# Kernel tuning notes

Hardware: AMD Instinct MI355X
Metric: run time of the kernel (lower is better)

The kernel has to match this reference:

```python
import jax, jax.numpy as jnp
import numpy as np

N_EMBED = 8192
EMBED_DIM = 64
BETA = 0.25


def setup_inputs() -> dict:
    key = jax.random.key(0)
    k_z, k_e = jax.random.split(key)
    z = jax.random.normal(k_z, (16, 4096, EMBED_DIM), dtype=jnp.float32)
    # embedding.weight.data.uniform_(-1/n_embed, 1/n_embed)
    embedding = jax.random.uniform(
        k_e, (N_EMBED, EMBED_DIM), dtype=jnp.float32,
        minval=-1.0 / N_EMBED, maxval=1.0 / N_EMBED)
    return {"z": z, "embedding": embedding}


def reference(z, embedding):
    # z: [B, H, C] with C == embed_dim (no permute needed)
    B, H, C = z.shape
    z_flat = z.reshape(-1, C)                      # [N, C]
    # squared euclidean distances: ||z||^2 + ||e||^2 - 2 z e^T
    d = (jnp.sum(z_flat ** 2, axis=1, keepdims=True)
         + jnp.sum(embedding ** 2, axis=1)
         - 2.0 * jnp.matmul(z_flat, embedding.T))  # [N, n_embed]
    idx = jnp.argmin(d, axis=1)                    # [N]
    z_q = embedding[idx].reshape(z.shape)          # gather + reshape
    sg = jax.lax.stop_gradient
    loss = (jnp.mean((sg(z_q) - z) ** 2)
            + BETA * jnp.mean((z_q - sg(z)) ** 2))
    # straight-through estimator
    z_q = z + sg(z_q - z)
    return z_q, loss, idx.reshape(B, H)
```

## Files before the change

### kernel.cpp

```cpp
#include <hip/hip_runtime.h>

typedef __attribute__((ext_vector_type(8))) short short8;
typedef __attribute__((ext_vector_type(16))) float floatx16;
typedef unsigned int u32;
typedef unsigned short u16;
typedef unsigned long long u64;

#define NROWS 65536
#define NEMB 8192
#define DIM 64
#define LOSS_OFF ((size_t)NROWS * DIM)
#define IDX_OFF (LOSS_OFF + 1)
#define CAPQ 16
#define CSTRIDE 66
#define NPRE 4
#define NSTAGE 64

#define WS_EFRAG_OFF 0u
#define WS_LPART_OFF (1u << 20)
#define WS_QUEUE_OFF ((1u << 20) + 8192u)
#define WS_QCNT_OFF  ((1u << 20) + 8192u + (256u << 10))
#define WS_LOVR_OFF  (WS_QCNT_OFF + 4u)
#define WS_NEED      (WS_QCNT_OFF + 64u)

typedef const __attribute__((address_space(1))) unsigned int GU32;
typedef __attribute__((address_space(3))) unsigned int LU32;

__device__ __forceinline__ unsigned short f2bf(float f) {
    u32 x = __float_as_uint(f);
    return (unsigned short)((x + 0x7fffu + ((x >> 16) & 1u)) >> 16);
}

__device__ __forceinline__ float zsum_np(const float* zf) {
    float r[8];
#pragma unroll
    for (int j = 0; j < 8; ++j) r[j] = zf[j] * zf[j];
#pragma unroll
    for (int i = 8; i < 64; i += 8) {
#pragma unroll
        for (int j = 0; j < 8; ++j) r[j] += zf[i + j] * zf[i + j];
    }
    return ((r[0] + r[1]) + (r[2] + r[3])) + ((r[4] + r[5]) + (r[6] + r[7]));
}

__device__ __forceinline__ float dot_chain(const float* zf, const float* e) {
    float acc = 0.f;
#pragma unroll
    for (int i = 0; i < 16; ++i) {
        float4 ev = ((const float4*)e)[i];
        acc = fmaf(zf[4 * i + 0], ev.x, acc);
        acc = fmaf(zf[4 * i + 1], ev.y, acc);
        acc = fmaf(zf[4 * i + 2], ev.z, acc);
        acc = fmaf(zf[4 * i + 3], ev.w, acc);
    }
    return acc;
}

__device__ __forceinline__ float vmax16_3(const floatx16& a) {
    float m0 = fmaxf(fmaxf(a[0], a[1]), a[2]);
    float m1 = fmaxf(fmaxf(a[3], a[4]), a[5]);
    float m2 = fmaxf(fmaxf(a[6], a[7]), a[8]);
    float m3 = fmaxf(fmaxf(a[9], a[10]), a[11]);
    float m4 = fmaxf(fmaxf(a[12], a[13]), a[14]);
    float n0 = fmaxf(fmaxf(m0, m1), m2);
    float n1 = fmaxf(fmaxf(m3, m4), a[15]);
    return fmaxf(n0, n1);
}

extern "C" __global__ __launch_bounds__(256)
void vq_prep(const float* __restrict__ emb, u32* __restrict__ efrag,
             u32* __restrict__ qcount, float* __restrict__ loss_over) {
    int tid = blockIdx.x * 256 + threadIdx.x;
    int t = tid >> 8, kc = (tid >> 5) & 7, m = tid & 31;
    const float* e = emb + (((size_t)t * 32 + m) * 64 + kc * 8);
    float4 a = ((const float4*)e)[0];
    float4 b = ((const float4*)e)[1];
    u32 w0 = (u32)f2bf(a.x) | ((u32)f2bf(a.y) << 16);
    u32 w1 = (u32)f2bf(a.z) | ((u32)f2bf(a.w) << 16);
    u32 w2 = (u32)f2bf(b.x) | ((u32)f2bf(b.y) << 16);
    u32 w3 = (u32)f2bf(b.z) | ((u32)f2bf(b.w) << 16);
    ((uint4*)efrag)[tid] = make_uint4(w0, w1, w2, w3);
    if (tid == 0) { qcount[0] = 0u; *loss_over = 0.f; }
}

extern "C" __global__ __launch_bounds__(256, 2)
void vq_screen(const float* __restrict__ z, const u32* __restrict__ efrag,
               const float* __restrict__ emb, float* __restrict__ out,
               float* __restrict__ lpart, u32* __restrict__ queue,
               u32* __restrict__ qcount) {
    __shared__ u32 etile[8192];
    __shared__ u16 cand[128 * CSTRIDE];
    __shared__ u32 cnt_l[512];
    __shared__ float runm_sh[128][2];
    __shared__ u32 win[128];
    __shared__ float lsum[4];
    const int tid = threadIdx.x;
    const int wave = tid >> 6, lane = tid & 63;
    const int rlo = lane & 31, h = lane >> 5;
    const int rowbase = blockIdx.x * 128 + (wave >> 1) * 64;
    const int sub = (wave & 1) * 2 + h;
    const int wp = wave & 1;

    if (tid < 128) { runm_sh[tid][0] = -3.4e38f; runm_sh[tid][1] = -3.4e38f; }

    {
        const u32* g = efrag + tid * 4;
        u32* l = etile + tid * 4;
#pragma unroll
        for (int r = 0; r < 4; ++r)
            __builtin_amdgcn_global_load_lds((GU32*)(g + r * 1024),
                                             (LU32*)(l + r * 1024), 16, 0, 0);
    }

    short8 zfr[2][4];
    float eps_[2];
#pragma unroll
    for (int rt = 0; rt < 2; ++rt) {
        const float* zp = z + (size_t)(rowbase + rt * 32 + rlo) * 64;
        float sa = 0.f;
#pragma unroll
        for (int s = 0; s < 4; ++s) {
            const float4* p = (const float4*)(zp + s * 16 + h * 8);
            float4 a = p[0], b = p[1];
            union { short8 v; unsigned short e[8]; } u;
            u.e[0] = f2bf(a.x); u.e[1] = f2bf(a.y);
            u.e[2] = f2bf(a.z); u.e[3] = f2bf(a.w);
            u.e[4] = f2bf(b.x); u.e[5] = f2bf(b.y);
            u.e[6] = f2bf(b.z); u.e[7] = f2bf(b.w);
            zfr[rt][s] = u.v;
            sa += fabsf(a.x) + fabsf(a.y) + fabsf(a.z) + fabsf(a.w)
                + fabsf(b.x) + fabsf(b.y) + fabsf(b.z) + fabsf(b.w);
        }
        sa += __shfl_xor(sa, 32);
        eps_[rt] = fmaf(1.1e-6f, sa, 1e-7f);
    }
    float runm[2] = { -3.4e38f, -3.4e38f };
    u32 pc[2] = { 0u, 0u };

    __syncthreads();
    int cur = 0;

    for (int ss = 0; ss < NSTAGE + NPRE; ++ss) {
        const int t = (ss < NPRE) ? ss : (ss - NPRE);

        {
            const int sn = ss + 1;
            if (sn < NSTAGE + NPRE) {
                const int tn = (sn < NPRE) ? sn : (sn - NPRE);
                const u32* g = efrag + (size_t)tn * 4096 + tid * 4;
                u32* l = etile + (cur ^ 1) * 4096 + tid * 4;
#pragma unroll
                for (int r = 0; r < 4; ++r)
                    __builtin_amdgcn_global_load_lds((GU32*)(g + r * 1024),
                                                     (LU32*)(l + r * 1024), 16, 0, 0);
            }
        }

#pragma unroll
        for (int rt = 0; rt < 2; ++rt) {
            const int rowl = (wave >> 1) * 64 + rt * 32 + rlo;
            runm[rt] = fmaxf(runm[rt], runm_sh[rowl][wp ^ 1]);
        }

        floatx16 acc[2][2];
#pragma unroll
        for (int et = 0; et < 2; ++et)
#pragma unroll
            for (int rt = 0; rt < 2; ++rt) acc[et][rt] = 0.f;

#pragma unroll
        for (int s = 0; s < 4; ++s) {
            short8 af[2];
#pragma unroll
            for (int et = 0; et < 2; ++et) {
                int off = cur * 16384 + (wp * 2 + et) * 4096 + (2 * s + h) * 512 + rlo * 16;
                af[et] = *(const short8*)((const char*)etile + off);
            }
#pragma unroll
            for (int et = 0; et < 2; ++et)
#pragma unroll
                for (int rt = 0; rt < 2; ++rt)
                    acc[et][rt] = __builtin_amdgcn_mfma_f32_32x32x16_bf16(
                        af[et], zfr[rt][s], acc[et][rt], 0, 0, 0);
        }

#pragma unroll
        for (int rt = 0; rt < 2; ++rt) {
            const int rowl = (wave >> 1) * 64 + rt * 32 + rlo;
            float vm[2];
#pragma unroll
            for (int et = 0; et < 2; ++et) vm[et] = vmax16_3(acc[et][rt]);
            float m64 = fmaxf(vm[0], vm[1]);
            runm[rt] = fmaxf(runm[rt], m64);
            runm[rt] = fmaxf(runm[rt], __shfl_xor(runm[rt], 32));
            if (ss >= NPRE) {
                const float thr = runm[rt] - eps_[rt];
                if (m64 >= thr) {
                    const int ebase = t * 128 + wp * 64;
                    const u32 cbase = (u32)rowl * CSTRIDE + (u32)sub * CAPQ;
#pragma unroll
                    for (int et = 0; et < 2; ++et) {
                        if (vm[et] >= thr) {
#pragma unroll
                            for (int r = 0; r < 16; ++r) {
                                float v = acc[et][rt][r];
                                if (v >= thr) {
                                    int j = ebase + et * 32 + ((r & 3) + 8 * (r >> 2) + 4 * h);
                                    if (pc[rt] < CAPQ) cand[cbase + pc[rt]] = (u16)j;
                                    pc[rt]++;
                                }
                            }
                        }
                    }
                }
            }
            if (h == 0) runm_sh[rowl][wp] = runm[rt];
        }

        __syncthreads();
        cur ^= 1;
    }
#pragma unroll
    for (int rt = 0; rt < 2; ++rt)
        cnt_l[(((wave >> 1) * 64 + rt * 32 + rlo) << 2) + sub] = pc[rt];
    __syncthreads();

    {
        const int rl = lane & 31, half = lane >> 5;
        const int rowl = wave * 32 + rl;
        const int grow = blockIdx.x * 128 + rowl;
        const u32 ca = cnt_l[(rowl << 2) + 2 * half];
        const u32 cb = cnt_l[(rowl << 2) + 2 * half + 1];
        u32 ovf = (u32)((ca > CAPQ) | (cb > CAPQ));
        ovf |= (u32)__shfl_xor((int)ovf, 32);

        if (!ovf) {
            float zf[64];
            const float4* zp = (const float4*)(z + (size_t)grow * 64);
#pragma unroll
            for (int i = 0; i < 16; ++i) {
                float4 a = zp[i];
                zf[4 * i + 0] = a.x; zf[4 * i + 1] = a.y;
                zf[4 * i + 2] = a.z; zf[4 * i + 3] = a.w;
            }
            const float zs = zsum_np(zf);
            u64 best = ~0ull;
            const u32 cbase = (u32)rowl * CSTRIDE + (u32)(2 * half) * CAPQ;
            for (u32 s = 0; s < ca; ++s) {
                u32 j = (u32)cand[cbase + s];
                float d = fmaf(-2.f, dot_chain(zf, emb + (size_t)j * 64), zs);
                u64 p = ((u64)__float_as_uint(d) << 32) | (u64)j;
                best = p < best ? p : best;
            }
            for (u32 s = 0; s < cb; ++s) {
                u32 j = (u32)cand[cbase + CAPQ + s];
                float d = fmaf(-2.f, dot_chain(zf, emb + (size_t)j * 64), zs);
                u64 p = ((u64)__float_as_uint(d) << 32) | (u64)j;
                best = p < best ? p : best;
            }
            u64 o = __shfl_xor(best, 32);
            best = o < best ? o : best;
            if (half == 0) {
                win[rowl] = (u32)best;
                out[IDX_OFF + grow] = (float)(u32)best;
            }
        } else if (half == 0) {
            u32 pos = atomicAdd(qcount, 1u);
            queue[pos] = (u32)grow;
            win[rowl] = 0xFFFFFFFFu;
        }
    }
    __syncthreads();

    float lp = 0.f;
    {
        const int r2 = tid >> 1, hf = tid & 1;
        const int grow2 = blockIdx.x * 128 + r2;
        const u32 wj = win[r2];
        if (wj != 0xFFFFFFFFu) {
            const float4* ep = (const float4*)(emb + (size_t)wj * 64) + hf * 8;
            const float4* zp4 = (const float4*)(z + (size_t)grow2 * 64) + hf * 8;
            float4* oq = (float4*)(out + (size_t)grow2 * 64) + hf * 8;
#pragma unroll
            for (int i = 0; i < 8; ++i) {
                float4 ev = ep[i];
                float4 zv = zp4[i];
                oq[i] = ev;
                float dx = ev.x - zv.x, dy = ev.y - zv.y;
                float dzv = ev.z - zv.z, dw = ev.w - zv.w;
                lp = fmaf(dx, dx, fmaf(dy, dy, fmaf(dzv, dzv, fmaf(dw, dw, lp))));
            }
        }
    }
#pragma unroll
    for (int off = 32; off; off >>= 1) lp += __shfl_down(lp, off);
    if (lane == 0) lsum[wave] = lp;
    __syncthreads();
    if (tid == 0)
        lpart[blockIdx.x] = (lsum[0] + lsum[1]) + (lsum[2] + lsum[3]);
}

extern "C" __global__ __launch_bounds__(256)
void vq_over(const float* __restrict__ z, const float* __restrict__ emb,
             const u32* __restrict__ queue, const u32* __restrict__ qcount,
             float* __restrict__ out, float* __restrict__ loss_over) {
    __shared__ u64 red[4];
    const int tid = threadIdx.x, wave = tid >> 6, lane = tid & 63;
    u32 n = qcount[0]; if (n > (u32)NROWS) n = (u32)NROWS;
    for (u32 qi = blockIdx.x; qi < n; qi += gridDim.x) {
        const int row = (int)queue[qi];
        const float4* zp = (const float4*)(z + (size_t)row * 64);
        float zf[64];
#pragma unroll
        for (int i = 0; i < 16; ++i) {
            float4 a = zp[i];
            zf[4 * i + 0] = a.x; zf[4 * i + 1] = a.y;
            zf[4 * i + 2] = a.z; zf[4 * i + 3] = a.w;
        }
        const float zs = zsum_np(zf);
        u64 best = ~0ull;
#pragma unroll 2
        for (int j = tid; j < NEMB; j += 256) {
            float d = fmaf(-2.f, dot_chain(zf, emb + (size_t)j * 64), zs);
            u64 p = ((u64)__float_as_uint(d) << 32) | (u64)j;
            best = p < best ? p : best;
        }
#pragma unroll
        for (int off = 32; off; off >>= 1) {
            u64 o = __shfl_xor(best, off);
            best = o < best ? o : best;
        }
        if (lane == 0) red[wave] = best;
        __syncthreads();
        if (tid == 0) {
            u64 b = red[0];
#pragma unroll
            for (int w = 1; w < 4; ++w) { u64 o = red[w]; b = o < b ? o : b; }
            red[0] = b;
            out[IDX_OFF + row] = (float)(u32)b;
        }
        __syncthreads();
        const u32 wj = (u32)red[0];
        float lp = 0.f;
        if (tid < 16) {
            float4 ev = ((const float4*)(emb + (size_t)wj * 64))[tid];
            float4 zv = zp[tid];
            ((float4*)(out + (size_t)row * 64))[tid] = ev;
            float dx = ev.x - zv.x, dy = ev.y - zv.y;
            float dzv = ev.z - zv.z, dw = ev.w - zv.w;
            lp = fmaf(dx, dx, fmaf(dy, dy, fmaf(dzv, dzv, dw * dw)));
        }
        if (wave == 0) {
#pragma unroll
            for (int off = 32; off; off >>= 1) lp += __shfl_down(lp, off);
            if (tid == 0) atomicAdd(loss_over, lp);
        }
        __syncthreads();
    }
}

extern "C" __global__ __launch_bounds__(256)
void vq_lossred(const float* __restrict__ lpart,
                const float* __restrict__ loss_over, float* __restrict__ out) {
    __shared__ float s[256];
    const int tid = threadIdx.x;
    float v = 0.f;
    for (int i = tid; i < 512; i += 256) v += lpart[i];
    s[tid] = v; __syncthreads();
    for (int off = 128; off; off >>= 1) {
        if (tid < off) s[tid] += s[tid + off];
        __syncthreads();
    }
    if (tid == 0) out[LOSS_OFF] = 1.25f * (s[0] + *loss_over) / 4194304.f;
}

extern "C" __global__ __launch_bounds__(256, 2)
void vq_legacy(const float* __restrict__ z, const float* __restrict__ emb,
               float* __restrict__ out, float* __restrict__ ws) {
    __shared__ float tile[128 * 64];
    __shared__ float red_d[4][128];
    __shared__ int   red_i[4][128];
    const int tid = threadIdx.x, lane = tid & 63, wave = tid >> 6;
    const int r0 = blockIdx.x * 128 + lane;
    float z0f[64], z1f[64];
    {
        const float4* p0 = (const float4*)(z + (size_t)r0 * 64);
        const float4* p1 = (const float4*)(z + ((size_t)r0 + 64) * 64);
#pragma unroll
        for (int i = 0; i < 16; ++i) {
            float4 a = p0[i];
            z0f[4*i+0]=a.x; z0f[4*i+1]=a.y; z0f[4*i+2]=a.z; z0f[4*i+3]=a.w;
            float4 b = p1[i];
            z1f[4*i+0]=b.x; z1f[4*i+1]=b.y; z1f[4*i+2]=b.z; z1f[4*i+3]=b.w;
        }
    }
    const float zs0 = zsum_np(z0f), zs1 = zsum_np(z1f);
    float bd0 = 3.402823466e38f, bd1 = 3.402823466e38f;
    int bi0 = 0, bi1 = 0;
    for (int t = 0; t < 64; ++t) {
        __syncthreads();
        {
            const float4* src = (const float4*)(emb + (size_t)t * 128 * 64);
            float4* dst = (float4*)tile;
#pragma unroll
            for (int i = 0; i < 8; ++i) dst[tid + i * 256] = src[tid + i * 256];
        }
        __syncthreads();
        const int base = wave * 32;
#pragma unroll 2
        for (int jg = 0; jg < 32; jg += 4) {
            const float* e = tile + (size_t)(base + jg) * 64;
            float a00=0,a10=0,a20=0,a30=0,a01=0,a11=0,a21=0,a31=0;
#pragma unroll
            for (int i = 0; i < 16; ++i) {
                float4 ea = ((const float4*)(e))[i];
                float4 eb = ((const float4*)(e + 64))[i];
                float4 ec = ((const float4*)(e + 128))[i];
                float4 ed = ((const float4*)(e + 192))[i];
                float x0=z0f[4*i],x1=z0f[4*i+1],x2=z0f[4*i+2],x3=z0f[4*i+3];
                float y0=z1f[4*i],y1=z1f[4*i+1],y2=z1f[4*i+2],y3=z1f[4*i+3];
                a00=fmaf(x0,ea.x,a00);a00=fmaf(x1,ea.y,a00);a00=fmaf(x2,ea.z,a00);a00=fmaf(x3,ea.w,a00);
                a10=fmaf(x0,eb.x,a10);a10=fmaf(x1,eb.y,a10);a10=fmaf(x2,eb.z,a10);a10=fmaf(x3,eb.w,a10);
                a20=fmaf(x0,ec.x,a20);a20=fmaf(x1,ec.y,a20);a20=fmaf(x2,ec.z,a20);a20=fmaf(x3,ec.w,a20);
                a30=fmaf(x0,ed.x,a30);a30=fmaf(x1,ed.y,a30);a30=fmaf(x2,ed.z,a30);a30=fmaf(x3,ed.w,a30);
                a01=fmaf(y0,ea.x,a01);a01=fmaf(y1,ea.y,a01);a01=fmaf(y2,ea.z,a01);a01=fmaf(y3,ea.w,a01);
                a11=fmaf(y0,eb.x,a11);a11=fmaf(y1,eb.y,a11);a11=fmaf(y2,eb.z,a11);a11=fmaf(y3,eb.w,a11);
                a21=fmaf(y0,ec.x,a21);a21=fmaf(y1,ec.y,a21);a21=fmaf(y2,ec.z,a21);a21=fmaf(y3,ec.w,a21);
                a31=fmaf(y0,ed.x,a31);a31=fmaf(y1,ed.y,a31);a31=fmaf(y2,ed.z,a31);a31=fmaf(y3,ed.w,a31);
            }
            const int gj = t * 128 + base + jg;
            float d;
            d=fmaf(-2.f,a00,zs0); if(d<bd0){bd0=d;bi0=gj;}
            d=fmaf(-2.f,a10,zs0); if(d<bd0){bd0=d;bi0=gj+1;}
            d=fmaf(-2.f,a20,zs0); if(d<bd0){bd0=d;bi0=gj+2;}
            d=fmaf(-2.f,a30,zs0); if(d<bd0){bd0=d;bi0=gj+3;}
            d=fmaf(-2.f,a01,zs1); if(d<bd1){bd1=d;bi1=gj;}
            d=fmaf(-2.f,a11,zs1); if(d<bd1){bd1=d;bi1=gj+1;}
            d=fmaf(-2.f,a21,zs1); if(d<bd1){bd1=d;bi1=gj+2;}
            d=fmaf(-2.f,a31,zs1); if(d<bd1){bd1=d;bi1=gj+3;}
        }
    }
    red_d[wave][lane]=bd0; red_i[wave][lane]=bi0;
    red_d[wave][lane+64]=bd1; red_i[wave][lane+64]=bi1;
    __syncthreads();
    if (wave == 0) {
        float blk = 0.f;
#pragma unroll
        for (int half = 0; half < 2; ++half) {
            const int lrow = lane + half * 64;
            const float* zrf = half ? z1f : z0f;
            float bd = red_d[0][lrow]; int bi = red_i[0][lrow];
#pragma unroll
            for (int w = 1; w < 4; ++w) {
                float dd = red_d[w][lrow]; int ii = red_i[w][lrow];
                if (dd < bd || (dd == bd && ii < bi)) { bd = dd; bi = ii; }
            }
            const size_t row = (size_t)blockIdx.x * 128 + lrow;
            out[IDX_OFF + row] = (float)bi;
            const float4* ep = (const float4*)(emb + (size_t)bi * 64);
            float4* oq = (float4*)(out + row * 64);
            float ls = 0.f;
#pragma unroll
            for (int i = 0; i < 16; ++i) {
                float4 ev = ep[i];
                oq[i] = ev;
                float dx=ev.x-zrf[4*i], dy=ev.y-zrf[4*i+1];
                float dzv=ev.z-zrf[4*i+2], dw=ev.w-zrf[4*i+3];
                ls=fmaf(dx,dx,ls); ls=fmaf(dy,dy,ls); ls=fmaf(dzv,dzv,ls); ls=fmaf(dw,dw,ls);
            }
            blk += ls;
        }
#pragma unroll
        for (int off = 32; off; off >>= 1) blk += __shfl_down(blk, off);
        if (lane == 0) ws[blockIdx.x] = blk;
    }
}

extern "C" __global__ __launch_bounds__(512)
void vq_legacy_loss(const float* __restrict__ ws, float* __restrict__ out) {
    __shared__ float s[8];
    const int tid = threadIdx.x;
    float v = ws[tid];
#pragma unroll
    for (int off = 32; off; off >>= 1) v += __shfl_down(v, off);
    if ((tid & 63) == 0) s[tid >> 6] = v;
    __syncthreads();
    if (tid == 0) {
        float t = 0.f;
#pragma unroll
        for (int i = 0; i < 8; ++i) t += s[i];
        out[LOSS_OFF] = 1.25f * t / 4194304.f;
    }
}

extern "C" void kernel_launch(void* const* d_in, const int* in_sizes, int n_in,
                              void* d_out, int out_size, void* d_ws, size_t ws_size,
                              hipStream_t stream) {
    const float* z   = (const float*)d_in[0];
    const float* emb = (const float*)d_in[1];
    float* out = (float*)d_out;
    if (ws_size < (size_t)WS_NEED) {
        float* ws = (float*)d_ws;
        vq_legacy<<<512, 256, 0, stream>>>(z, emb, out, ws);
        vq_legacy_loss<<<1, 512, 0, stream>>>(ws, out);
        return;
    }
    char* wsb = (char*)d_ws;
    u32* efrag = (u32*)(wsb + WS_EFRAG_OFF);
    float* lpart = (float*)(wsb + WS_LPART_OFF);
    u32* queue   = (u32*)(wsb + WS_QUEUE_OFF);
    u32* qcount  = (u32*)(wsb + WS_QCNT_OFF);
    float* loss_over = (float*)(wsb + WS_LOVR_OFF);
    vq_prep<<<256, 256, 0, stream>>>(emb, efrag, qcount, loss_over);
    vq_screen<<<512, 256, 0, stream>>>(z, efrag, emb, out, lpart, queue, qcount);
    vq_over<<<256, 256, 0, stream>>>(z, emb, queue, qcount, out, loss_over);
    vq_lossred<<<1, 256, 0, stream>>>(lpart, loss_over, out);
}
```

Before: 217.6 us.

## Split codebook across two blocks per row tile with atomicMin merge

The screening kernel now splits the 8192-entry codebook into two halves, each handled by a separate block (1024 blocks), and merges per-row winners with 64-bit atomicMin into a workspace array. The etile double buffer is replaced by a single buffer with syncs before and after each load, which cuts LDS so four blocks can fit per CU. A new vq_final kernel does the gather, output and loss, and overflow rows are rescanned per half. The aim is more parallelism and occupancy, paid for with an extra launch, atomics, duplicate z loads and loss of load/compute overlap in the staging loop.

```diff
diff --git a/kernel.cpp b/kernel.cpp
--- a/kernel.cpp
+++ b/kernel.cpp
@@ -14,13 +14,13 @@
 #define CAPQ 16
 #define CSTRIDE 66
 #define NPRE 4
-#define NSTAGE 64
+#define NSTAGE 32
 
 #define WS_EFRAG_OFF 0u
-#define WS_LPART_OFF (1u << 20)
-#define WS_QUEUE_OFF ((1u << 20) + 8192u)
-#define WS_QCNT_OFF  ((1u << 20) + 8192u + (256u << 10))
-#define WS_LOVR_OFF  (WS_QCNT_OFF + 4u)
+#define WS_BEST_OFF  (1u << 20)
+#define WS_QUEUE_OFF ((1u << 20) + (512u << 10))
+#define WS_LPART_OFF (WS_QUEUE_OFF + (512u << 10))
+#define WS_QCNT_OFF  (WS_LPART_OFF + 8192u)
 #define WS_NEED      (WS_QCNT_OFF + 64u)
 
 typedef const __attribute__((address_space(1))) unsigned int GU32;
@@ -69,7 +69,7 @@
 
 extern "C" __global__ __launch_bounds__(256)
 void vq_prep(const float* __restrict__ emb, u32* __restrict__ efrag,
-             u32* __restrict__ qcount, float* __restrict__ loss_over) {
+             u64* __restrict__ best, u32* __restrict__ qcount) {
     int tid = blockIdx.x * 256 + threadIdx.x;
     int t = tid >> 8, kc = (tid >> 5) & 7, m = tid & 31;
     const float* e = emb + (((size_t)t * 32 + m) * 64 + kc * 8);
@@ -80,37 +80,28 @@
     u32 w2 = (u32)f2bf(b.x) | ((u32)f2bf(b.y) << 16);
     u32 w3 = (u32)f2bf(b.z) | ((u32)f2bf(b.w) << 16);
     ((uint4*)efrag)[tid] = make_uint4(w0, w1, w2, w3);
-    if (tid == 0) { qcount[0] = 0u; *loss_over = 0.f; }
-}
-
-extern "C" __global__ __launch_bounds__(256, 2)
+    best[tid] = ~0ull;
+    if (tid == 0) qcount[0] = 0u;
+}
+
+extern "C" __global__ __launch_bounds__(256, 4)
 void vq_screen(const float* __restrict__ z, const u32* __restrict__ efrag,
-               const float* __restrict__ emb, float* __restrict__ out,
-               float* __restrict__ lpart, u32* __restrict__ queue,
-               u32* __restrict__ qcount) {
-    __shared__ u32 etile[8192];
+               const float* __restrict__ emb, u64* __restrict__ best,
+               u32* __restrict__ queue, u32* __restrict__ qcount) {
+    __shared__ u32 etile[4096];
     __shared__ u16 cand[128 * CSTRIDE];
     __shared__ u32 cnt_l[512];
     __shared__ float runm_sh[128][2];
-    __shared__ u32 win[128];
-    __shared__ float lsum[4];
     const int tid = threadIdx.x;
     const int wave = tid >> 6, lane = tid & 63;
     const int rlo = lane & 31, h = lane >> 5;
-    const int rowbase = blockIdx.x * 128 + (wave >> 1) * 64;
+    const int rowblk = blockIdx.x >> 1, halfid = blockIdx.x & 1;
+    const int rowbase = rowblk * 128 + (wave >> 1) * 64;
     const int sub = (wave & 1) * 2 + h;
     const int wp = wave & 1;
+    const u32 halfu = (u32)halfid * 131072u;
 
     if (tid < 128) { runm_sh[tid][0] = -3.4e38f; runm_sh[tid][1] = -3.4e38f; }
-
-    {
-        const u32* g = efrag + tid * 4;
-        u32* l = etile + tid * 4;
-#pragma unroll
-        for (int r = 0; r < 4; ++r)
-            __builtin_amdgcn_global_load_lds((GU32*)(g + r * 1024),
-                                             (LU32*)(l + r * 1024), 16, 0, 0);
-    }
 
     short8 zfr[2][4];
     float eps_[2];
@@ -137,24 +128,18 @@
     float runm[2] = { -3.4e38f, -3.4e38f };
     u32 pc[2] = { 0u, 0u };
 
-    __syncthreads();
-    int cur = 0;
-
     for (int ss = 0; ss < NSTAGE + NPRE; ++ss) {
         const int t = (ss < NPRE) ? ss : (ss - NPRE);
-
+        __syncthreads();
         {
-            const int sn = ss + 1;
-            if (sn < NSTAGE + NPRE) {
-                const int tn = (sn < NPRE) ? sn : (sn - NPRE);
-                const u32* g = efrag + (size_t)tn * 4096 + tid * 4;
-                u32* l = etile + (cur ^ 1) * 4096 + tid * 4;
-#pragma unroll
-                for (int r = 0; r < 4; ++r)
-                    __builtin_amdgcn_global_load_lds((GU32*)(g + r * 1024),
-                                                     (LU32*)(l + r * 1024), 16, 0, 0);
-            }
-        }
+            const u32* g = efrag + halfu + (u32)t * 4096u + tid * 4;
+            u32* l = etile + tid * 4;
+#pragma unroll
+            for (int r = 0; r < 4; ++r)
+                __builtin_amdgcn_global_load_lds((GU32*)(g + r * 1024),
+                                                 (LU32*)(l + r * 1024), 16, 0, 0);
+        }
+        __syncthreads();
 
 #pragma unroll
         for (int rt = 0; rt < 2; ++rt) {
@@ -173,7 +158,7 @@
             short8 af[2];
 #pragma unroll
             for (int et = 0; et < 2; ++et) {
-                int off = cur * 16384 + (wp * 2 + et) * 4096 + (2 * s + h) * 512 + rlo * 16;
+                int off = (wp * 2 + et) * 4096 + (2 * s + h) * 512 + rlo * 16;
                 af[et] = *(const short8*)((const char*)etile + off);
             }
 #pragma unroll
@@ -196,7 +181,7 @@
             if (ss >= NPRE) {
                 const float thr = runm[rt] - eps_[rt];
                 if (m64 >= thr) {
-                    const int ebase = t * 128 + wp * 64;
+                    const int ebase = halfid * 4096 + t * 128 + wp * 64;
                     const u32 cbase = (u32)rowl * CSTRIDE + (u32)sub * CAPQ;
 #pragma unroll
                     for (int et = 0; et < 2; ++et) {
@@ -216,9 +201,6 @@
             }
             if (h == 0) runm_sh[rowl][wp] = runm[rt];
         }
-
-        __syncthreads();
-        cur ^= 1;
     }
 #pragma unroll
     for (int rt = 0; rt < 2; ++rt)
@@ -228,7 +210,7 @@
     {
         const int rl = lane & 31, half = lane >> 5;
         const int rowl = wave * 32 + rl;
-        const int grow = blockIdx.x * 128 + rowl;
+        const int grow = rowblk * 128 + rowl;
         const u32 ca = cnt_l[(rowl << 2) + 2 * half];
         const u32 cb = cnt_l[(rowl << 2) + 2 * half + 1];
         u32 ovf = (u32)((ca > CAPQ) | (cb > CAPQ));
@@ -244,52 +226,98 @@
                 zf[4 * i + 2] = a.z; zf[4 * i + 3] = a.w;
             }
             const float zs = zsum_np(zf);
-            u64 best = ~0ull;
+            u64 b = ~0ull;
             const u32 cbase = (u32)rowl * CSTRIDE + (u32)(2 * half) * CAPQ;
             for (u32 s = 0; s < ca; ++s) {
                 u32 j = (u32)cand[cbase + s];
                 float d = fmaf(-2.f, dot_chain(zf, emb + (size_t)j * 64), zs);
                 u64 p = ((u64)__float_as_uint(d) << 32) | (u64)j;
-                best = p < best ? p : best;
+                b = p < b ? p : b;
             }
             for (u32 s = 0; s < cb; ++s) {
                 u32 j = (u32)cand[cbase + CAPQ + s];
                 float d = fmaf(-2.f, dot_chain(zf, emb + (size_t)j * 64), zs);
                 u64 p = ((u64)__float_as_uint(d) << 32) | (u64)j;
-                best = p < best ? p : best;
-            }
-            u64 o = __shfl_xor(best, 32);
-            best = o < best ? o : best;
-            if (half == 0) {
-                win[rowl] = (u32)best;
-                out[IDX_OFF + grow] = (float)(u32)best;
-            }
+                b = p < b ? p : b;
+            }
+            u64 o = __shfl_xor(b, 32);
+            b = o < b ? o : b;
+            if (half == 0) atomicMin(&best[grow], b);
         } else if (half == 0) {
             u32 pos = atomicAdd(qcount, 1u);
-            queue[pos] = (u32)grow;
-            win[rowl] = 0xFFFFFFFFu;
-        }
-    }
-    __syncthreads();
-
+            queue[pos] = (u32)grow | ((u32)halfid << 16);
+        }
+    }
+}
+
+extern "C" __global__ __launch_bounds__(256)
+void vq_over(const float* __restrict__ z, const float* __restrict__ emb,
+             const u32* __restrict__ queue, const u32* __restrict__ qcount,
+             u64* __restrict__ best) {
+    __shared__ u64 red[4];
+    const int tid = threadIdx.x, wave = tid >> 6, lane = tid & 63;
+    u32 n = qcount[0]; if (n > 2u * (u32)NROWS) n = 2u * (u32)NROWS;
+    for (u32 qi = blockIdx.x; qi < n; qi += gridDim.x) {
+        const u32 e = queue[qi];
+        const int row = (int)(e & 0xFFFFu);
+        const int hb = (int)((e >> 16) & 1u) * 4096;
+        const float4* zp = (const float4*)(z + (size_t)row * 64);
+        float zf[64];
+#pragma unroll
+        for (int i = 0; i < 16; ++i) {
+            float4 a = zp[i];
+            zf[4 * i + 0] = a.x; zf[4 * i + 1] = a.y;
+            zf[4 * i + 2] = a.z; zf[4 * i + 3] = a.w;
+        }
+        const float zs = zsum_np(zf);
+        u64 b = ~0ull;
+#pragma unroll 2
+        for (int j = tid; j < 4096; j += 256) {
+            const int gj = hb + j;
+            float d = fmaf(-2.f, dot_chain(zf, emb + (size_t)gj * 64), zs);
+            u64 p = ((u64)__float_as_uint(d) << 32) | (u64)gj;
+            b = p < b ? p : b;
+        }
+#pragma unroll
+        for (int off = 32; off; off >>= 1) {
+            u64 o = __shfl_xor(b, off);
+            b = o < b ? o : b;
+        }
+        if (lane == 0) red[wave] = b;
+        __syncthreads();
+        if (tid == 0) {
+            u64 bb = red[0];
+#pragma unroll
+            for (int w = 1; w < 4; ++w) { u64 o = red[w]; bb = o < bb ? o : bb; }
+            atomicMin(&best[row], bb);
+        }
+        __syncthreads();
+    }
+}
+
+extern "C" __global__ __launch_bounds__(256)
+void vq_final(const float* __restrict__ z, const float* __restrict__ emb,
+              const u64* __restrict__ best, float* __restrict__ out,
+              float* __restrict__ lpart) {
+    __shared__ float lsum[4];
+    const int tid = threadIdx.x, wave = tid >> 6, lane = tid & 63;
+    const int r2 = tid >> 1, hf = tid & 1;
+    const int grow = blockIdx.x * 128 + r2;
+    const u32 wj = (u32)best[grow];
+    if (hf == 0) out[IDX_OFF + grow] = (float)wj;
     float lp = 0.f;
     {
-        const int r2 = tid >> 1, hf = tid & 1;
-        const int grow2 = blockIdx.x * 128 + r2;
-        const u32 wj = win[r2];
-        if (wj != 0xFFFFFFFFu) {
-            const float4* ep = (const float4*)(emb + (size_t)wj * 64) + hf * 8;
-            const float4* zp4 = (const float4*)(z + (size_t)grow2 * 64) + hf * 8;
-            float4* oq = (float4*)(out + (size_t)grow2 * 64) + hf * 8;
-#pragma unroll
-            for (int i = 0; i < 8; ++i) {
-                float4 ev = ep[i];
-                float4 zv = zp4[i];
-                oq[i] = ev;
-                float dx = ev.x - zv.x, dy = ev.y - zv.y;
-                float dzv = ev.z - zv.z, dw = ev.w - zv.w;
-                lp = fmaf(dx, dx, fmaf(dy, dy, fmaf(dzv, dzv, fmaf(dw, dw, lp))));
-            }
+        const float4* ep = (const float4*)(emb + (size_t)wj * 64) + hf * 8;
+        const float4* zp4 = (const float4*)(z + (size_t)grow * 64) + hf * 8;
+        float4* oq = (float4*)(out + (size_t)grow * 64) + hf * 8;
+#pragma unroll
+        for (int i = 0; i < 8; ++i) {
+            float4 ev = ep[i];
+            float4 zv = zp4[i];
+            oq[i] = ev;
+            float dx = ev.x - zv.x, dy = ev.y - zv.y;
+            float dzv = ev.z - zv.z, dw = ev.w - zv.w;
+            lp = fmaf(dx, dx, fmaf(dy, dy, fmaf(dzv, dzv, fmaf(dw, dw, lp))));
         }
     }
 #pragma unroll
@@ -301,67 +329,7 @@
 }
 
 extern "C" __global__ __launch_bounds__(256)
-void vq_over(const float* __restrict__ z, const float* __restrict__ emb,
-             const u32* __restrict__ queue, const u32* __restrict__ qcount,
-             float* __restrict__ out, float* __restrict__ loss_over) {
-    __shared__ u64 red[4];
-    const int tid = threadIdx.x, wave = tid >> 6, lane = tid & 63;
-    u32 n = qcount[0]; if (n > (u32)NROWS) n = (u32)NROWS;
-    for (u32 qi = blockIdx.x; qi < n; qi += gridDim.x) {
-        const int row = (int)queue[qi];
-        const float4* zp = (const float4*)(z + (size_t)row * 64);
-        float zf[64];
-#pragma unroll
-        for (int i = 0; i < 16; ++i) {
-            float4 a = zp[i];
-            zf[4 * i + 0] = a.x; zf[4 * i + 1] = a.y;
-            zf[4 * i + 2] = a.z; zf[4 * i + 3] = a.w;
-        }
-        const float zs = zsum_np(zf);
-        u64 best = ~0ull;
-#pragma unroll 2
-        for (int j = tid; j < NEMB; j += 256) {
-            float d = fmaf(-2.f, dot_chain(zf, emb + (size_t)j * 64), zs);
-            u64 p = ((u64)__float_as_uint(d) << 32) | (u64)j;
-            best = p < best ? p : best;
-        }
-#pragma unroll
-        for (int off = 32; off; off >>= 1) {
-            u64 o = __shfl_xor(best, off);
-            best = o < best ? o : best;
-        }
-        if (lane == 0) red[wave] = best;
-        __syncthreads();
-        if (tid == 0) {
-            u64 b = red[0];
-#pragma unroll
-            for (int w = 1; w < 4; ++w) { u64 o = red[w]; b = o < b ? o : b; }
-            red[0] = b;
-            out[IDX_OFF + row] = (float)(u32)b;
-        }
-        __syncthreads();
-        const u32 wj = (u32)red[0];
-        float lp = 0.f;
-        if (tid < 16) {
-            float4 ev = ((const float4*)(emb + (size_t)wj * 64))[tid];
-            float4 zv = zp[tid];
-            ((float4*)(out + (size_t)row * 64))[tid] = ev;
-            float dx = ev.x - zv.x, dy = ev.y - zv.y;
-            float dzv = ev.z - zv.z, dw = ev.w - zv.w;
-            lp = fmaf(dx, dx, fmaf(dy, dy, fmaf(dzv, dzv, dw * dw)));
-        }
-        if (wave == 0) {
-#pragma unroll
-            for (int off = 32; off; off >>= 1) lp += __shfl_down(lp, off);
-            if (tid == 0) atomicAdd(loss_over, lp);
-        }
-        __syncthreads();
-    }
-}
-
-extern "C" __global__ __launch_bounds__(256)
-void vq_lossred(const float* __restrict__ lpart,
-                const float* __restrict__ loss_over, float* __restrict__ out) {
+void vq_lossred(const float* __restrict__ lpart, float* __restrict__ out) {
     __shared__ float s[256];
     const int tid = threadIdx.x;
     float v = 0.f;
@@ -371,7 +339,7 @@
         if (tid < off) s[tid] += s[tid + off];
         __syncthreads();
     }
-    if (tid == 0) out[LOSS_OFF] = 1.25f * (s[0] + *loss_over) / 4194304.f;
+    if (tid == 0) out[LOSS_OFF] = 1.25f * s[0] / 4194304.f;
 }
 
 extern "C" __global__ __launch_bounds__(256, 2)
@@ -506,13 +474,14 @@
         return;
     }
     char* wsb = (char*)d_ws;
-    u32* efrag = (u32*)(wsb + WS_EFRAG_OFF);
+    u32* efrag   = (u32*)(wsb + WS_EFRAG_OFF);
+    u64* best    = (u64*)(wsb + WS_BEST_OFF);
+    u32* queue   = (u32*)(wsb + WS_QUEUE_OFF);
     float* lpart = (float*)(wsb + WS_LPART_OFF);
-    u32* queue   = (u32*)(wsb + WS_QUEUE_OFF);
     u32* qcount  = (u32*)(wsb + WS_QCNT_OFF);
-    float* loss_over = (float*)(wsb + WS_LOVR_OFF);
-    vq_prep<<<256, 256, 0, stream>>>(emb, efrag, qcount, loss_over);
-    vq_screen<<<512, 256, 0, stream>>>(z, efrag, emb, out, lpart, queue, qcount);
-    vq_over<<<256, 256, 0, stream>>>(z, emb, queue, qcount, out, loss_over);
-    vq_lossred<<<1, 256, 0, stream>>>(lpart, loss_over, out);
-}
+    vq_prep<<<256, 256, 0, stream>>>(emb, efrag, best, qcount);
+    vq_screen<<<1024, 256, 0, stream>>>(z, efrag, emb, best, queue, qcount);
+    vq_over<<<256, 256, 0, stream>>>(z, emb, queue, qcount, best);
+    vq_final<<<512, 256, 0, stream>>>(z, emb, best, out, lpart);
+    vq_lossred<<<1, 256, 0, stream>>>(lpart, out);
+}
```

After: 201.8 us. 1.08x faster.
